# Performance work log

Measured on AMD Instinct MI355X. Metric: run time of the kernel, lower is better.

## Reference

```python
import jax, jax.numpy as jnp
import numpy as np
from jax import lax

H, N, L = 256, 64, 4096
DT_MIN, DT_MAX = 0.001, 0.1


def make_hippo(n_state):
    n = jnp.arange(n_state)
    P = jnp.sqrt(1.0 + 2.0 * n)
    A = P[:, None] * P[None, :]
    A = jnp.tril(A) - jnp.diag(n.astype(jnp.float32))
    B = jnp.sqrt(2.0 * n + 1.0)[:, None]
    return -A, B


def setup_inputs() -> dict:
    key = jax.random.key(0)
    A, B = make_hippo(N)
    A = jnp.broadcast_to(A, (H, N, N))            # H N N
    B = jnp.broadcast_to(B, (H, N, 1))            # H N 1
    log_dt = jnp.linspace(DT_MIN, DT_MAX, H)      # note: used directly as dt (as in source)
    u = jax.random.normal(key, (L,), dtype=jnp.float32)
    return {"u": u, "A": A, "B": B, "log_dt": log_dt}


def reference(u, A, B, log_dt):
    dt = log_dt  # `.dt` property returns log_dt.value unchanged
    I = jnp.eye(N, dtype=A.dtype)
    dt2A = (dt[:, None, None] * 0.5) * A                      # H N N
    BL = jnp.linalg.inv(I - dt2A)                             # H N N (batched inv)
    Ab = BL @ (I + dt2A)                                      # H N N
    Bb = (BL * dt[:, None, None]) @ B                         # H N 1

    # Bb * u broadcast: L H N
    Bb_u = u[:, None, None] * Bb[None, :, :, 0]

    def step(x, b_k):
        x1 = jnp.einsum('hnm,hm->hn', Ab, x) + b_k            # H N
        return x1, x1

    state0 = jnp.zeros((H, N), dtype=u.dtype)
    _, x = lax.scan(step, state0, Bb_u)                       # x: L H N
    return x
```

## Files before the change

### kernel.cpp

```cpp
#include <hip/hip_runtime.h>

#define NHEAD 256

typedef _Float16 f16x8 __attribute__((ext_vector_type(8)));
typedef float f32x4 __attribute__((ext_vector_type(4)));

__device__ __forceinline__ int mel(int r, int c) {
  return (r << 6) + ((((c >> 3) ^ r) & 7) << 3) + (c & 7);
}
__device__ __forceinline__ f16x8 ldfrag(const _Float16* M, int r, int u) {
  return *(const f16x8*)(M + (r << 6) + (((u ^ r) & 7) << 3));
}
__device__ __forceinline__ f32x4 MF(f16x8 a, f16x8 b, f32x4 c) {
  return __builtin_amdgcn_mfma_f32_16x16x32_f16(a, b, c, 0, 0, 0);
}

__device__ __forceinline__ void mmstep8(const _Float16* A, int ar0,
                                        const _Float16* BT, _Float16* Dr,
                                        _Float16* Dt, int dr0, int nrb, int w,
                                        int c15, int g) {
  const int wc = w & 3;
  f16x8 b0 = ldfrag(BT, (wc << 4) + c15, g);
  f16x8 b1 = ldfrag(BT, (wc << 4) + c15, 4 + g);
  for (int ib = (w >> 2); ib < nrb; ib += 2) {
    f32x4 acc = {0.f, 0.f, 0.f, 0.f};
    f16x8 a0 = ldfrag(A, ar0 + (ib << 4) + c15, g);
    f16x8 a1 = ldfrag(A, ar0 + (ib << 4) + c15, 4 + g);
    acc = MF(a0, b0, acc);
    acc = MF(a1, b1, acc);
#pragma unroll
    for (int j = 0; j < 4; ++j) {
      const int rr = dr0 + (ib << 4) + (g << 2) + j;
      const int cc = (wc << 4) + c15;
      const _Float16 v = (_Float16)acc[j];
      Dr[mel(rr, cc)] = v;
      Dt[mel(cc, rr)] = v;
    }
  }
}

__global__ __launch_bounds__(512, 2) void hippo_fused(
    const float* __restrict__ u, const float* __restrict__ Ag,
    const float* __restrict__ Bv, const float* __restrict__ dtv,
    float* __restrict__ out) {
  const int h = blockIdx.x;
  const int t = threadIdx.x;
  const int w = t >> 6;
  const int lane = t & 63;
  const int c15 = lane & 15;
  const int g = lane >> 4;

  __shared__ __align__(16) _Float16 URV[4 * 4616];
  __shared__ __align__(16) _Float16 RING[4 * 4096];
  __shared__ __align__(16) char UNI[49152];
  __shared__ __align__(16) _Float16 PB23[2 * 4096];
  __shared__ float RED[8][68];
  __shared__ float KC[64];

  float* Ms = (float*)UNI;
  float* Xs = (float*)(UNI + 16384);
  float* invd = (float*)(UNI + 16384 + 17408);
  _Float16* PB0 = (_Float16*)UNI;
  _Float16* PB1 = PB0 + 4096;
  _Float16* PB4 = (_Float16*)(UNI + 16384);
  _Float16* PB5 = PB4 + 4096;
  _Float16* PB2 = PB23;
  _Float16* PB3 = PB23 + 4096;

  for (int s = 0; s < 4; ++s)
    for (int x = t; x < 4616; x += 512) {
      const int q = 4095 - x - s;
      URV[s * 4616 + x] = (q >= 0) ? (_Float16)u[q] : (_Float16)0.f;
    }
  const float dt = dtv[h];
  const float* Ah = Ag + (size_t)h * 4096;
  for (int idx = t; idx < 4096; idx += 512) {
    const int r = idx >> 6, c = idx & 63;
    const float a = Ah[idx];
    const float half = 0.5f * dt * a;
    const float id = (r == c) ? 1.0f : 0.0f;
    Ms[r * 64 + c] = id - half;
    Xs[r * 68 + c] = id + half;
  }
  if (t < 64) {
    Xs[t * 68 + 64] = dt * Bv[h * 64 + t];
    Xs[t * 68 + 65] = 0.f;
    Xs[t * 68 + 66] = 0.f;
    Xs[t * 68 + 67] = 0.f;
    invd[t] = 1.0f / (1.0f - 0.5f * dt * Ah[t * 65]);
  }
  __syncthreads();

  for (int k = 0; k < 64; k += 4) {
    if (t < 68) {
      const int c = t;
      const float x0 = Xs[k * 68 + c] * invd[k];
      const float x1 = (Xs[(k + 1) * 68 + c] - Ms[(k + 1) * 64 + k] * x0) * invd[k + 1];
      const float x2 = (Xs[(k + 2) * 68 + c] - Ms[(k + 2) * 64 + k] * x0 -
                        Ms[(k + 2) * 64 + k + 1] * x1) * invd[k + 2];
      const float x3 = (Xs[(k + 3) * 68 + c] - Ms[(k + 3) * 64 + k] * x0 -
                        Ms[(k + 3) * 64 + k + 1] * x1 -
                        Ms[(k + 3) * 64 + k + 2] * x2) * invd[k + 3];
      Xs[k * 68 + c] = x0;
      Xs[(k + 1) * 68 + c] = x1;
      Xs[(k + 2) * 68 + c] = x2;
      Xs[(k + 3) * 68 + c] = x3;
    }
    __syncthreads();
    const int nwork = (60 - k) * 17;
    for (int idx = t; idx < nwork; idx += 512) {
      const int r = k + 4 + idx / 17;
      const int cu = (idx % 17) * 4;
      float4 xr = *(float4*)&Xs[r * 68 + cu];
      const float m0 = Ms[r * 64 + k], m1 = Ms[r * 64 + k + 1];
      const float m2 = Ms[r * 64 + k + 2], m3 = Ms[r * 64 + k + 3];
      const float4 a0 = *(float4*)&Xs[k * 68 + cu];
      const float4 a1 = *(float4*)&Xs[(k + 1) * 68 + cu];
      const float4 a2 = *(float4*)&Xs[(k + 2) * 68 + cu];
      const float4 a3 = *(float4*)&Xs[(k + 3) * 68 + cu];
      xr.x -= m0 * a0.x + m1 * a1.x + m2 * a2.x + m3 * a3.x;
      xr.y -= m0 * a0.y + m1 * a1.y + m2 * a2.y + m3 * a3.y;
      xr.z -= m0 * a0.z + m1 * a1.z + m2 * a2.z + m3 * a3.z;
      xr.w -= m0 * a0.w + m1 * a1.w + m2 * a2.w + m3 * a3.w;
      *(float4*)&Xs[r * 68 + cu] = xr;
    }
    __syncthreads();
  }

  for (int idx = t; idx < 4096; idx += 512) {
    const int r = idx >> 6, cc = idx & 63;
    const _Float16 v = (_Float16)Xs[r * 68 + cc];
    PB0[mel(r, cc)] = v;
    PB1[mel(cc, r)] = v;
  }
  if (t < 64) {
    const float bb = Xs[t * 68 + 64];
    KC[t] = bb;
    PB2[mel(0, t)] = (_Float16)bb;
    PB3[mel(t, 0)] = (_Float16)bb;
  }
  __syncthreads();

  {
    const int mrow = t & 63, q = w;
    for (int d = 1; d < 16; ++d) {
      const float4* ar = (const float4*)(Xs + mrow * 68 + q * 8);
      const float4 av0 = ar[0], av1 = ar[1];
      const int jb = q * 8;
      RED[q][mrow] = av0.x * KC[jb] + av0.y * KC[jb + 1] + av0.z * KC[jb + 2] +
                     av0.w * KC[jb + 3] + av1.x * KC[jb + 4] + av1.y * KC[jb + 5] +
                     av1.z * KC[jb + 6] + av1.w * KC[jb + 7];
      __syncthreads();
      if (t < 64) {
        float s2 = 0.f;
#pragma unroll
        for (int qq = 0; qq < 8; ++qq) s2 += RED[qq][t];
        KC[t] = s2;
        PB2[mel(d, t)] = (_Float16)s2;
        PB3[mel(t, d)] = (_Float16)s2;
      }
      __syncthreads();
    }
  }

  mmstep8(PB0, 0, PB1, PB4, PB5, 0, 4, w, c15, g); __syncthreads();
  mmstep8(PB4, 0, PB5, PB0, PB1, 0, 4, w, c15, g); __syncthreads();
  mmstep8(PB0, 0, PB1, PB4, PB5, 0, 4, w, c15, g); __syncthreads();
  mmstep8(PB4, 0, PB5, PB0, PB1, 0, 4, w, c15, g); __syncthreads();
  mmstep8(PB0, 0, PB1, PB4, PB5, 0, 4, w, c15, g); __syncthreads();
  mmstep8(PB2, 0, PB0, PB2, PB3, 16, 1, w, c15, g); __syncthreads();
  mmstep8(PB2, 0, PB4, PB2, PB3, 32, 2, w, c15, g); __syncthreads();
  mmstep8(PB4, 0, PB5, PB0, PB1, 0, 4, w, c15, g); __syncthreads();

  f16x8 bt[8][4];
  f16x8 bc[2][4];
  auto LB = [&](f16x8* dst, const _Float16* BT, int kk) {
#pragma unroll
    for (int nb = 0; nb < 4; ++nb)
      dst[nb] = ldfrag(BT, (nb << 4) + c15, (kk << 2) + g);
  };

  LB(bt[0], PB3, 0); LB(bt[1], PB3, 1);
  mmstep8(PB2, 0, PB0, PB4, PB5, 0, 4, w, c15, g); __syncthreads();
  LB(bt[2], PB5, 0); LB(bt[3], PB5, 1);
  mmstep8(PB4, 0, PB0, PB2, PB3, 0, 4, w, c15, g); __syncthreads();
  LB(bt[4], PB3, 0); LB(bt[5], PB3, 1);
  mmstep8(PB2, 0, PB0, PB4, PB5, 0, 4, w, c15, g); __syncthreads();
  LB(bt[6], PB5, 0); LB(bt[7], PB5, 1);
  mmstep8(PB1, 0, PB0, PB2, PB3, 0, 4, w, c15, g); __syncthreads();
  mmstep8(PB2, 0, PB3, PB4, PB1, 0, 4, w, c15, g); __syncthreads();
  LB(bc[0], PB1, 0); LB(bc[1], PB1, 1);
  __syncthreads();

  const int chain = w & 3;
  const int half = w >> 2;
  _Float16* ringw = RING + (chain << 12);
  float* outh = out + (h << 6);
  const int lanebase = (g << 3) - c15;

#pragma unroll 1
  for (int mstep = 0; mstep < 16; ++mstep) {
    const int c = chain + (mstep << 2);
    f32x4 acc[2][4];
#pragma unroll
    for (int ibl = 0; ibl < 2; ++ibl)
#pragma unroll
      for (int nb = 0; nb < 4; ++nb) acc[ibl][nb] = f32x4{0.f, 0.f, 0.f, 0.f};

#pragma unroll
    for (int ks = 0; ks < 8; ++ks) {
      const int tt = ks >> 1;
      const int base = 4095 - 64 * (c - tt) + ((ks & 1) << 5) + lanebase;
#pragma unroll
      for (int ibl = 0; ibl < 2; ++ibl) {
        const int ib = (half << 1) + ibl;
        const int m0 = base - (ib << 4);
        const int lo = m0 & 3;
        const uint2* p = (const uint2*)(URV + lo * 4616 + (m0 - lo));
        union { f16x8 hv; uint2 u2[2]; } ua;
        ua.u2[0] = p[0];
        ua.u2[1] = p[1];
#pragma unroll
        for (int nb = 0; nb < 4; ++nb)
          acc[ibl][nb] = MF(ua.hv, bt[ks][nb], acc[ibl][nb]);
      }
    }
    if (mstep > 0) {
#pragma unroll
      for (int kk = 0; kk < 2; ++kk)
#pragma unroll
        for (int ibl = 0; ibl < 2; ++ibl) {
          const int row = (((half << 1) + ibl) << 4) + c15;
          const f16x8 a = ldfrag(ringw, row, (kk << 2) + g);
#pragma unroll
          for (int nb = 0; nb < 4; ++nb)
            acc[ibl][nb] = MF(a, bc[kk][nb], acc[ibl][nb]);
        }
    }
    const int ob = c << 6;
#pragma unroll
    for (int ibl = 0; ibl < 2; ++ibl)
#pragma unroll
      for (int nb = 0; nb < 4; ++nb) {
        const int n = (nb << 4) + c15;
#pragma unroll
        for (int j = 0; j < 4; ++j) {
          const int i = (((half << 1) + ibl) << 4) + (g << 2) + j;
          const float v = acc[ibl][nb][j];
          ringw[mel(i, n)] = (_Float16)v;
          outh[(size_t)(ob + i) * 16384 + n] = v;
        }
      }
  }
}

extern "C" void kernel_launch(void* const* d_in, const int* in_sizes, int n_in,
                              void* d_out, int out_size, void* d_ws,
                              size_t ws_size, hipStream_t stream) {
  const float* u = (const float*)d_in[0];
  const float* A = (const float*)d_in[1];
  const float* B = (const float*)d_in[2];
  const float* dt = (const float*)d_in[3];
  float* out = (float*)d_out;
  hippo_fused<<<dim3(NHEAD), dim3(512), 0, stream>>>(u, A, B, dt, out);
}
```

Before: 73.78 us.

## Stage outputs through swizzled LDS for vector stores; doubling-based power precompute

```diff
diff --git a/kernel.cpp b/kernel.cpp
--- a/kernel.cpp
+++ b/kernel.cpp
@@ -15,26 +15,29 @@
   return __builtin_amdgcn_mfma_f32_16x16x32_f16(a, b, c, 0, 0, 0);
 }
 
-__device__ __forceinline__ void mmstep8(const _Float16* A, int ar0,
-                                        const _Float16* BT, _Float16* Dr,
-                                        _Float16* Dt, int dr0, int nrb, int w,
-                                        int c15, int g) {
+__device__ __forceinline__ void mmstep8(const _Float16* A, const _Float16* BT,
+                                        _Float16* Dr, _Float16* Dt, int dr0,
+                                        int nrb, int limit, int w, int c15,
+                                        int g) {
   const int wc = w & 3;
   f16x8 b0 = ldfrag(BT, (wc << 4) + c15, g);
   f16x8 b1 = ldfrag(BT, (wc << 4) + c15, 4 + g);
   for (int ib = (w >> 2); ib < nrb; ib += 2) {
     f32x4 acc = {0.f, 0.f, 0.f, 0.f};
-    f16x8 a0 = ldfrag(A, ar0 + (ib << 4) + c15, g);
-    f16x8 a1 = ldfrag(A, ar0 + (ib << 4) + c15, 4 + g);
+    f16x8 a0 = ldfrag(A, (ib << 4) + c15, g);
+    f16x8 a1 = ldfrag(A, (ib << 4) + c15, 4 + g);
     acc = MF(a0, b0, acc);
     acc = MF(a1, b1, acc);
 #pragma unroll
     for (int j = 0; j < 4; ++j) {
-      const int rr = dr0 + (ib << 4) + (g << 2) + j;
-      const int cc = (wc << 4) + c15;
-      const _Float16 v = (_Float16)acc[j];
-      Dr[mel(rr, cc)] = v;
-      Dt[mel(cc, rr)] = v;
+      const int lr = (ib << 4) + (g << 2) + j;
+      if (lr < limit) {
+        const int rr = dr0 + lr;
+        const int cc = (wc << 4) + c15;
+        const _Float16 v = (_Float16)acc[j];
+        Dr[mel(rr, cc)] = v;
+        Dt[mel(cc, rr)] = v;
+      }
     }
   }
 }
@@ -54,7 +57,7 @@
   __shared__ __align__(16) _Float16 RING[4 * 4096];
   __shared__ __align__(16) char UNI[49152];
   __shared__ __align__(16) _Float16 PB23[2 * 4096];
-  __shared__ float RED[8][68];
+  __shared__ float RED[8][64];
   __shared__ float KC[64];
 
   float* Ms = (float*)UNI;
@@ -77,10 +80,10 @@
   for (int idx = t; idx < 4096; idx += 512) {
     const int r = idx >> 6, c = idx & 63;
     const float a = Ah[idx];
-    const float half = 0.5f * dt * a;
+    const float half_ = 0.5f * dt * a;
     const float id = (r == c) ? 1.0f : 0.0f;
-    Ms[r * 64 + c] = id - half;
-    Xs[r * 68 + c] = id + half;
+    Ms[r * 64 + c] = id - half_;
+    Xs[r * 68 + c] = id + half_;
   }
   if (t < 64) {
     Xs[t * 68 + 64] = dt * Bv[h * 64 + t];
@@ -142,35 +145,35 @@
   __syncthreads();
 
   {
-    const int mrow = t & 63, q = w;
-    for (int d = 1; d < 16; ++d) {
-      const float4* ar = (const float4*)(Xs + mrow * 68 + q * 8);
-      const float4 av0 = ar[0], av1 = ar[1];
-      const int jb = q * 8;
-      RED[q][mrow] = av0.x * KC[jb] + av0.y * KC[jb + 1] + av0.z * KC[jb + 2] +
-                     av0.w * KC[jb + 3] + av1.x * KC[jb + 4] + av1.y * KC[jb + 5] +
-                     av1.z * KC[jb + 6] + av1.w * KC[jb + 7];
-      __syncthreads();
-      if (t < 64) {
-        float s2 = 0.f;
-#pragma unroll
-        for (int qq = 0; qq < 8; ++qq) s2 += RED[qq][t];
-        KC[t] = s2;
-        PB2[mel(d, t)] = (_Float16)s2;
-        PB3[mel(t, d)] = (_Float16)s2;
-      }
-      __syncthreads();
-    }
-  }
-
-  mmstep8(PB0, 0, PB1, PB4, PB5, 0, 4, w, c15, g); __syncthreads();
-  mmstep8(PB4, 0, PB5, PB0, PB1, 0, 4, w, c15, g); __syncthreads();
-  mmstep8(PB0, 0, PB1, PB4, PB5, 0, 4, w, c15, g); __syncthreads();
-  mmstep8(PB4, 0, PB5, PB0, PB1, 0, 4, w, c15, g); __syncthreads();
-  mmstep8(PB0, 0, PB1, PB4, PB5, 0, 4, w, c15, g); __syncthreads();
-  mmstep8(PB2, 0, PB0, PB2, PB3, 16, 1, w, c15, g); __syncthreads();
-  mmstep8(PB2, 0, PB4, PB2, PB3, 32, 2, w, c15, g); __syncthreads();
-  mmstep8(PB4, 0, PB5, PB0, PB1, 0, 4, w, c15, g); __syncthreads();
+    const int mrow = t & 63;
+    const float4* ar = (const float4*)(Xs + mrow * 68 + w * 8);
+    const float4 av0 = ar[0], av1 = ar[1];
+    const int jb = w * 8;
+    RED[w][mrow] = av0.x * KC[jb] + av0.y * KC[jb + 1] + av0.z * KC[jb + 2] +
+                   av0.w * KC[jb + 3] + av1.x * KC[jb + 4] + av1.y * KC[jb + 5] +
+                   av1.z * KC[jb + 6] + av1.w * KC[jb + 7];
+    __syncthreads();
+    if (t < 64) {
+      float s2 = 0.f;
+#pragma unroll
+      for (int qq = 0; qq < 8; ++qq) s2 += RED[qq][t];
+      PB2[mel(1, t)] = (_Float16)s2;
+      PB3[mel(t, 1)] = (_Float16)s2;
+    }
+    __syncthreads();
+  }
+
+  mmstep8(PB0, PB1, PB4, PB5, 0, 4, 64, w, c15, g); __syncthreads();
+  mmstep8(PB2, PB4, PB2, PB3, 2, 1, 2, w, c15, g);  __syncthreads();
+  mmstep8(PB4, PB5, PB0, PB1, 0, 4, 64, w, c15, g); __syncthreads();
+  mmstep8(PB2, PB0, PB2, PB3, 4, 1, 4, w, c15, g);  __syncthreads();
+  mmstep8(PB0, PB1, PB4, PB5, 0, 4, 64, w, c15, g); __syncthreads();
+  mmstep8(PB2, PB4, PB2, PB3, 8, 1, 8, w, c15, g);  __syncthreads();
+  mmstep8(PB4, PB5, PB0, PB1, 0, 4, 64, w, c15, g); __syncthreads();
+  mmstep8(PB2, PB0, PB2, PB3, 16, 1, 16, w, c15, g); __syncthreads();
+  mmstep8(PB0, PB1, PB4, PB5, 0, 4, 64, w, c15, g); __syncthreads();
+  mmstep8(PB2, PB4, PB2, PB3, 32, 2, 32, w, c15, g); __syncthreads();
+  mmstep8(PB4, PB5, PB0, PB1, 0, 4, 64, w, c15, g); __syncthreads();
 
   f16x8 bt[8][4];
   f16x8 bc[2][4];
@@ -181,14 +184,14 @@
   };
 
   LB(bt[0], PB3, 0); LB(bt[1], PB3, 1);
-  mmstep8(PB2, 0, PB0, PB4, PB5, 0, 4, w, c15, g); __syncthreads();
+  mmstep8(PB2, PB0, PB4, PB5, 0, 4, 64, w, c15, g); __syncthreads();
   LB(bt[2], PB5, 0); LB(bt[3], PB5, 1);
-  mmstep8(PB4, 0, PB0, PB2, PB3, 0, 4, w, c15, g); __syncthreads();
+  mmstep8(PB4, PB0, PB2, PB3, 0, 4, 64, w, c15, g); __syncthreads();
   LB(bt[4], PB3, 0); LB(bt[5], PB3, 1);
-  mmstep8(PB2, 0, PB0, PB4, PB5, 0, 4, w, c15, g); __syncthreads();
+  mmstep8(PB2, PB0, PB4, PB5, 0, 4, 64, w, c15, g); __syncthreads();
   LB(bt[6], PB5, 0); LB(bt[7], PB5, 1);
-  mmstep8(PB1, 0, PB0, PB2, PB3, 0, 4, w, c15, g); __syncthreads();
-  mmstep8(PB2, 0, PB3, PB4, PB1, 0, 4, w, c15, g); __syncthreads();
+  mmstep8(PB1, PB0, PB2, PB3, 0, 4, 64, w, c15, g); __syncthreads();
+  mmstep8(PB2, PB3, PB4, PB1, 0, 4, 64, w, c15, g); __syncthreads();
   LB(bc[0], PB1, 0); LB(bc[1], PB1, 1);
   __syncthreads();
 
@@ -197,10 +200,22 @@
   _Float16* ringw = RING + (chain << 12);
   float* outh = out + (h << 6);
   const int lanebase = (g << 3) - c15;
+  float* OT = (w < 6) ? (float*)(UNI + w * 8192)
+                      : (float*)((char*)PB23 + (w - 6) * 8192);
+  int pc = -1;
 
 #pragma unroll 1
   for (int mstep = 0; mstep < 16; ++mstep) {
     const int c = chain + (mstep << 2);
+    if (mstep > 0) {
+#pragma unroll
+      for (int s = 0; s < 8; ++s) {
+        const int lr = (s << 2) + g;
+        const f32x4 v = *(const f32x4*)(OT + (lr << 6) + (((c15 ^ lr) & 15) << 2));
+        *(f32x4*)(outh + (size_t)((pc << 6) + (half << 5) + lr) * 16384 +
+                  (c15 << 2)) = v;
+      }
+    }
     f32x4 acc[2][4];
 #pragma unroll
     for (int ibl = 0; ibl < 2; ++ibl)
@@ -237,7 +252,6 @@
             acc[ibl][nb] = MF(a, bc[kk][nb], acc[ibl][nb]);
         }
     }
-    const int ob = c << 6;
 #pragma unroll
     for (int ibl = 0; ibl < 2; ++ibl)
 #pragma unroll
@@ -245,12 +259,19 @@
         const int n = (nb << 4) + c15;
 #pragma unroll
         for (int j = 0; j < 4; ++j) {
-          const int i = (((half << 1) + ibl) << 4) + (g << 2) + j;
+          const int lr = (ibl << 4) + (g << 2) + j;
           const float v = acc[ibl][nb][j];
-          ringw[mel(i, n)] = (_Float16)v;
-          outh[(size_t)(ob + i) * 16384 + n] = v;
+          ringw[mel((half << 5) + lr, n)] = (_Float16)v;
+          OT[(lr << 6) + ((((n >> 2) ^ lr) & 15) << 2) + (n & 3)] = v;
         }
       }
+    pc = c;
+  }
+#pragma unroll
+  for (int s = 0; s < 8; ++s) {
+    const int lr = (s << 2) + g;
+    const f32x4 v = *(const f32x4*)(OT + (lr << 6) + (((c15 ^ lr) & 15) << 2));
+    *(f32x4*)(outh + (size_t)((pc << 6) + (half << 5) + lr) * 16384 + (c15 << 2)) = v;
   }
 }
 
```

After: 186.1 us. 152% more time.
